# Optimization experiments

Measured on AMD Instinct MI355X. Metric: run time of the kernel, lower is better.

## Reference

```python
import jax, jax.numpy as jnp
import numpy as np

N = 50000
E = 800000
IN_DIM = 128
HID = 128


def setup_inputs() -> dict:
    key = jax.random.key(0)
    ks = jax.random.split(key, 8)
    x = jax.random.normal(ks[0], (N, IN_DIM), dtype=jnp.float32)
    edge_index = jax.random.randint(ks[1], (2, E), 0, N, dtype=jnp.int64)
    s1 = 1.0 / np.sqrt(IN_DIM)
    s2 = 1.0 / np.sqrt(HID)
    Wl1 = jax.random.uniform(ks[2], (HID, IN_DIM), jnp.float32, -s1, s1)
    bl1 = jnp.zeros((HID,), jnp.float32)
    Wr1 = jax.random.uniform(ks[3], (HID, IN_DIM), jnp.float32, -s1, s1)
    Wl2 = jax.random.uniform(ks[4], (HID, HID), jnp.float32, -s2, s2)
    bl2 = jnp.zeros((HID,), jnp.float32)
    Wr2 = jax.random.uniform(ks[5], (HID, HID), jnp.float32, -s2, s2)
    return {"x": x, "Wl1": Wl1, "bl1": bl1, "Wr1": Wr1,
            "Wl2": Wl2, "bl2": bl2, "Wr2": Wr2, "edge_index": edge_index}


def _sage_layer(h, src, dst, deg_inv, Wl, bl, Wr):
    # mean aggregation over in-edges: gather source feats, scatter-sum to targets
    msg_sum = jax.ops.segment_sum(h[src], dst, num_segments=N)  # [N, d]
    agg = msg_sum * deg_inv[:, None]
    return agg @ Wl.T + bl + h @ Wr.T


def reference(x, Wl1, bl1, Wr1, Wl2, bl2, Wr2, edge_index):
    src, dst = edge_index[0], edge_index[1]
    deg = jax.ops.segment_sum(jnp.ones((E,), x.dtype), dst, num_segments=N)
    deg_inv = 1.0 / jnp.maximum(deg, 1.0)
    h = jax.nn.relu(_sage_layer(x, src, dst, deg_inv, Wl1, bl1, Wr1))
    h = jax.nn.relu(_sage_layer(h, src, dst, deg_inv, Wl2, bl2, Wr2))
    return h  # dropout is identity in eval mode
```

## Files before the change

### kernel.cpp

```cpp
#include <hip/hip_runtime.h>

#define N_NODES 50000
#define N_ROWS_PAD 50064
#define N_EDGES 800000
#define DIM 128
#define KCAT 256
#define CAP 64

#define PACK_N (2 * DIM * KCAT)
#define CAST_N (N_NODES * 16)
#define FILL_N N_EDGES
#define PREP_TOTAL (PACK_N + CAST_N + FILL_N)

typedef unsigned int u32;
typedef unsigned short u16;
typedef __attribute__((ext_vector_type(8))) short short8;
typedef __attribute__((ext_vector_type(4))) float f32x4;

static __device__ __forceinline__ u16 f2bf(float f) {
  union { float f; u32 u; } v; v.f = f;
  u32 r = v.u + 0x7fffu + ((v.u >> 16) & 1u);
  return (u16)(r >> 16);
}
static __device__ __forceinline__ float bflo(u32 p) { return __uint_as_float(p << 16); }
static __device__ __forceinline__ float bfhi(u32 p) { return __uint_as_float(p & 0xffff0000u); }

__global__ void prep(const float* __restrict__ wl1, const float* __restrict__ wr1,
                     const float* __restrict__ wl2, const float* __restrict__ wr2,
                     const float* __restrict__ x,
                     const int* __restrict__ src, const int* __restrict__ dst,
                     int* __restrict__ cnt, u16* __restrict__ csr,
                     u16* __restrict__ wcat, u32* __restrict__ abuf) {
  int idx = blockIdx.x * blockDim.x + threadIdx.x;
  if (idx < PACK_N) {
    int layer = idx >> 15;
    int n = (idx >> 8) & 127;
    int k = idx & 255;
    const float* wl = layer ? wl2 : wl1;
    const float* wr = layer ? wr2 : wr1;
    float v = (k < DIM) ? wl[n * DIM + k] : wr[n * DIM + (k - DIM)];
    wcat[idx] = f2bf(v);
  } else if (idx < PACK_N + CAST_N) {
    int t = idx - PACK_N;
    int node = t >> 4, q = t & 15;
    float4 v0 = ((const float4*)x)[(size_t)node * 32 + q * 2];
    float4 v1 = ((const float4*)x)[(size_t)node * 32 + q * 2 + 1];
    uint4 p;
    p.x = (u32)f2bf(v0.x) | ((u32)f2bf(v0.y) << 16);
    p.y = (u32)f2bf(v0.z) | ((u32)f2bf(v0.w) << 16);
    p.z = (u32)f2bf(v1.x) | ((u32)f2bf(v1.y) << 16);
    p.w = (u32)f2bf(v1.z) | ((u32)f2bf(v1.w) << 16);
    ((uint4*)abuf)[(size_t)node * 32 + 16 + q] = p;
  } else {
    int e = idx - (PACK_N + CAST_N);
    if (e < N_EDGES) {
      int d = dst[e];
      int pos = atomicAdd(&cnt[d], 1);
      if (pos < CAP) csr[(size_t)pos * N_NODES + d] = (u16)src[e];
    }
  }
}

__global__ __launch_bounds__(256) void aggregate(
    u32* __restrict__ abuf, const u16* __restrict__ csr,
    const int* __restrict__ cnt) {
  int wid = (blockIdx.x * blockDim.x + threadIdx.x) >> 6;
  if (wid >= N_NODES) return;
  int lane = threadIdx.x & 63;
  int sub = lane >> 4, q = lane & 15;
  int craw = cnt[wid];
  int c = min(craw, CAP);
  const u16* col = csr + wid;
  const uint4* h16 = (const uint4*)abuf;
  float a0 = 0, a1 = 0, a2 = 0, a3 = 0, a4 = 0, a5 = 0, a6 = 0, a7 = 0;
#define ACC8(u) { a0 += bflo(u.x); a1 += bfhi(u.x); a2 += bflo(u.y); a3 += bfhi(u.y); \
                  a4 += bflo(u.z); a5 += bfhi(u.z); a6 += bflo(u.w); a7 += bfhi(u.w); }
  int i = sub;
  for (; i + 12 < c; i += 16) {
    u32 s0 = col[(size_t)i * N_NODES];
    u32 s1 = col[(size_t)(i + 4) * N_NODES];
    u32 s2 = col[(size_t)(i + 8) * N_NODES];
    u32 s3 = col[(size_t)(i + 12) * N_NODES];
    uint4 u0 = h16[(size_t)s0 * 32 + 16 + q];
    uint4 u1 = h16[(size_t)s1 * 32 + 16 + q];
    uint4 u2 = h16[(size_t)s2 * 32 + 16 + q];
    uint4 u3 = h16[(size_t)s3 * 32 + 16 + q];
    ACC8(u0); ACC8(u1); ACC8(u2); ACC8(u3);
  }
  for (; i < c; i += 4) {
    uint4 u0 = h16[(size_t)((u32)col[(size_t)i * N_NODES]) * 32 + 16 + q];
    ACC8(u0);
  }
#undef ACC8
  a0 += __shfl_xor(a0, 16); a1 += __shfl_xor(a1, 16);
  a2 += __shfl_xor(a2, 16); a3 += __shfl_xor(a3, 16);
  a4 += __shfl_xor(a4, 16); a5 += __shfl_xor(a5, 16);
  a6 += __shfl_xor(a6, 16); a7 += __shfl_xor(a7, 16);
  a0 += __shfl_xor(a0, 32); a1 += __shfl_xor(a1, 32);
  a2 += __shfl_xor(a2, 32); a3 += __shfl_xor(a3, 32);
  a4 += __shfl_xor(a4, 32); a5 += __shfl_xor(a5, 32);
  a6 += __shfl_xor(a6, 32); a7 += __shfl_xor(a7, 32);
  if (lane < 16) {
    float di = 1.0f / (float)max(craw, 1);
    uint4 p;
    p.x = (u32)f2bf(a0 * di) | ((u32)f2bf(a1 * di) << 16);
    p.y = (u32)f2bf(a2 * di) | ((u32)f2bf(a3 * di) << 16);
    p.z = (u32)f2bf(a4 * di) | ((u32)f2bf(a5 * di) << 16);
    p.w = (u32)f2bf(a6 * di) | ((u32)f2bf(a7 * di) << 16);
    ((uint4*)abuf)[(size_t)wid * 32 + q] = p;
  }
}

__global__ __launch_bounds__(256) void dense_mfma(
    const u16* __restrict__ abuf, const u16* __restrict__ wcat,
    const float* __restrict__ bias, float* __restrict__ fout,
    u16* __restrict__ bout) {
  const int lane = threadIdx.x & 63;
  const int wv = threadIdx.x >> 6;
  const int row0 = blockIdx.x * 64 + wv * 16;
  const int l15 = lane & 15;
  const int koff = (lane >> 4) * 8;

  const short8* ap = (const short8*)(abuf + (size_t)(row0 + l15) * KCAT + koff);
  const short8* bp = (const short8*)(wcat + (size_t)l15 * KCAT + koff);

  f32x4 acc[8];
#pragma unroll
  for (int t = 0; t < 8; ++t) acc[t] = (f32x4){0.f, 0.f, 0.f, 0.f};

#pragma unroll
  for (int ks = 0; ks < 8; ++ks) {
    short8 a = ap[ks * 4];
#pragma unroll
    for (int nt = 0; nt < 8; ++nt) {
      short8 b = bp[nt * 512 + ks * 4];
      acc[nt] = __builtin_amdgcn_mfma_f32_16x16x32_bf16(a, b, acc[nt], 0, 0, 0);
    }
  }

  const int rbase = row0 + ((lane >> 4) << 2);
#pragma unroll
  for (int nt = 0; nt < 8; ++nt) {
    int col = nt * 16 + l15;
    float bb = bias[col];
#pragma unroll
    for (int r = 0; r < 4; ++r) {
      int row = rbase + r;
      if (row < N_NODES) {
        float v = fmaxf(acc[nt][r] + bb, 0.f);
        if (fout) fout[(size_t)row * DIM + col] = v;
        if (bout) bout[(size_t)row * KCAT + DIM + col] = f2bf(v);
      }
    }
  }
}

extern "C" void kernel_launch(void* const* d_in, const int* in_sizes, int n_in,
                              void* d_out, int out_size, void* d_ws, size_t ws_size,
                              hipStream_t stream) {
  const float* x   = (const float*)d_in[0];
  const float* Wl1 = (const float*)d_in[1];
  const float* bl1 = (const float*)d_in[2];
  const float* Wr1 = (const float*)d_in[3];
  const float* Wl2 = (const float*)d_in[4];
  const float* bl2 = (const float*)d_in[5];
  const float* Wr2 = (const float*)d_in[6];
  const int* eidx  = (const int*)d_in[7];
  const int* src = eidx;
  const int* dst = eidx + N_EDGES;
  float* out = (float*)d_out;

  char* ws = (char*)d_ws;
  int* cnt  = (int*)ws;
  u16* csr  = (u16*)(ws + 256 * 1024);
  u16* wcat = (u16*)(ws + 6815744);
  u16* abuf = (u16*)(ws + 6946816);

  hipMemsetAsync(cnt, 0, N_NODES * sizeof(int), stream);

  prep<<<PREP_TOTAL / 256, 256, 0, stream>>>(Wl1, Wr1, Wl2, Wr2, x, src, dst,
                                             cnt, csr, wcat, (u32*)abuf);

  const int agg_grid = (N_NODES * 64 + 255) / 256;
  const int dense_grid = N_ROWS_PAD / 64;

  aggregate<<<agg_grid, 256, 0, stream>>>((u32*)abuf, csr, cnt);
  dense_mfma<<<dense_grid, 256, 0, stream>>>(abuf, wcat, bl1, (float*)nullptr, abuf);

  aggregate<<<agg_grid, 256, 0, stream>>>((u32*)abuf, csr, cnt);
  dense_mfma<<<dense_grid, 256, 0, stream>>>(abuf, wcat + DIM * KCAT, bl2, out,
                                             (u16*)nullptr);
}
```

Baseline: 271.0 us.

## Fuse neighbor aggregation into MFMA dense layer via shared-memory staging

Merges the aggregate and dense_mfma kernels into one fused_layer kernel. Each wavefront aggregates its 16 rows into LDS and then feeds them straight into the MFMA, so the aggregated half of the concatenated activation buffer no longer round-trips through global memory. Features are split into separate x and h buffers with a 128-wide pitch, and the CSR fill uses nontemporal stores. The cost is fewer waves in flight during the latency-bound gather: one wave now handles 16 nodes serially, where before each node had its own wave.

```diff
diff --git a/kernel.cpp b/kernel.cpp
--- a/kernel.cpp
+++ b/kernel.cpp
@@ -6,11 +6,11 @@
 #define DIM 128
 #define KCAT 256
 #define CAP 64
+#define MPITCH 264
 
 #define PACK_N (2 * DIM * KCAT)
 #define CAST_N (N_NODES * 16)
-#define FILL_N N_EDGES
-#define PREP_TOTAL (PACK_N + CAST_N + FILL_N)
+#define PREP_TOTAL (PACK_N + CAST_N + N_EDGES)
 
 typedef unsigned int u32;
 typedef unsigned short u16;
@@ -30,7 +30,7 @@
                      const float* __restrict__ x,
                      const int* __restrict__ src, const int* __restrict__ dst,
                      int* __restrict__ cnt, u16* __restrict__ csr,
-                     u16* __restrict__ wcat, u32* __restrict__ abuf) {
+                     u16* __restrict__ wcat, u32* __restrict__ bufx) {
   int idx = blockIdx.x * blockDim.x + threadIdx.x;
   if (idx < PACK_N) {
     int layer = idx >> 15;
@@ -50,106 +50,115 @@
     p.y = (u32)f2bf(v0.z) | ((u32)f2bf(v0.w) << 16);
     p.z = (u32)f2bf(v1.x) | ((u32)f2bf(v1.y) << 16);
     p.w = (u32)f2bf(v1.z) | ((u32)f2bf(v1.w) << 16);
-    ((uint4*)abuf)[(size_t)node * 32 + 16 + q] = p;
+    ((uint4*)bufx)[(size_t)node * 16 + q] = p;
   } else {
     int e = idx - (PACK_N + CAST_N);
     if (e < N_EDGES) {
       int d = dst[e];
       int pos = atomicAdd(&cnt[d], 1);
-      if (pos < CAP) csr[(size_t)pos * N_NODES + d] = (u16)src[e];
-    }
-  }
-}
-
-__global__ __launch_bounds__(256) void aggregate(
-    u32* __restrict__ abuf, const u16* __restrict__ csr,
-    const int* __restrict__ cnt) {
-  int wid = (blockIdx.x * blockDim.x + threadIdx.x) >> 6;
-  if (wid >= N_NODES) return;
-  int lane = threadIdx.x & 63;
-  int sub = lane >> 4, q = lane & 15;
-  int craw = cnt[wid];
-  int c = min(craw, CAP);
-  const u16* col = csr + wid;
-  const uint4* h16 = (const uint4*)abuf;
-  float a0 = 0, a1 = 0, a2 = 0, a3 = 0, a4 = 0, a5 = 0, a6 = 0, a7 = 0;
-#define ACC8(u) { a0 += bflo(u.x); a1 += bfhi(u.x); a2 += bflo(u.y); a3 += bfhi(u.y); \
-                  a4 += bflo(u.z); a5 += bfhi(u.z); a6 += bflo(u.w); a7 += bfhi(u.w); }
-  int i = sub;
-  for (; i + 12 < c; i += 16) {
-    u32 s0 = col[(size_t)i * N_NODES];
-    u32 s1 = col[(size_t)(i + 4) * N_NODES];
-    u32 s2 = col[(size_t)(i + 8) * N_NODES];
-    u32 s3 = col[(size_t)(i + 12) * N_NODES];
-    uint4 u0 = h16[(size_t)s0 * 32 + 16 + q];
-    uint4 u1 = h16[(size_t)s1 * 32 + 16 + q];
-    uint4 u2 = h16[(size_t)s2 * 32 + 16 + q];
-    uint4 u3 = h16[(size_t)s3 * 32 + 16 + q];
-    ACC8(u0); ACC8(u1); ACC8(u2); ACC8(u3);
-  }
-  for (; i < c; i += 4) {
-    uint4 u0 = h16[(size_t)((u32)col[(size_t)i * N_NODES]) * 32 + 16 + q];
-    ACC8(u0);
-  }
-#undef ACC8
-  a0 += __shfl_xor(a0, 16); a1 += __shfl_xor(a1, 16);
-  a2 += __shfl_xor(a2, 16); a3 += __shfl_xor(a3, 16);
-  a4 += __shfl_xor(a4, 16); a5 += __shfl_xor(a5, 16);
-  a6 += __shfl_xor(a6, 16); a7 += __shfl_xor(a7, 16);
-  a0 += __shfl_xor(a0, 32); a1 += __shfl_xor(a1, 32);
-  a2 += __shfl_xor(a2, 32); a3 += __shfl_xor(a3, 32);
-  a4 += __shfl_xor(a4, 32); a5 += __shfl_xor(a5, 32);
-  a6 += __shfl_xor(a6, 32); a7 += __shfl_xor(a7, 32);
-  if (lane < 16) {
-    float di = 1.0f / (float)max(craw, 1);
-    uint4 p;
-    p.x = (u32)f2bf(a0 * di) | ((u32)f2bf(a1 * di) << 16);
-    p.y = (u32)f2bf(a2 * di) | ((u32)f2bf(a3 * di) << 16);
-    p.z = (u32)f2bf(a4 * di) | ((u32)f2bf(a5 * di) << 16);
-    p.w = (u32)f2bf(a6 * di) | ((u32)f2bf(a7 * di) << 16);
-    ((uint4*)abuf)[(size_t)wid * 32 + q] = p;
-  }
-}
-
-__global__ __launch_bounds__(256) void dense_mfma(
-    const u16* __restrict__ abuf, const u16* __restrict__ wcat,
+      if (pos < CAP)
+        __builtin_nontemporal_store((u16)src[e], &csr[(size_t)pos * N_NODES + d]);
+    }
+  }
+}
+
+__global__ __launch_bounds__(256) void fused_layer(
+    const u16* __restrict__ hin, const u16* __restrict__ csr,
+    const int* __restrict__ cnt, const u16* __restrict__ wcat,
     const float* __restrict__ bias, float* __restrict__ fout,
     u16* __restrict__ bout) {
+  __shared__ u16 smsg[4 * 16 * MPITCH];
   const int lane = threadIdx.x & 63;
   const int wv = threadIdx.x >> 6;
   const int row0 = blockIdx.x * 64 + wv * 16;
+  const int sub = lane >> 4, q = lane & 15;
+  const uint4* h16 = (const uint4*)hin;
+  u16* msgw = smsg + wv * 16 * MPITCH;
+
+  for (int r = 0; r < 16; ++r) {
+    int node = row0 + r;
+    if (node >= N_NODES) break;
+    int craw = cnt[node];
+    int c = min(craw, CAP);
+    const u16* col = csr + node;
+    float a0 = 0, a1 = 0, a2 = 0, a3 = 0, a4 = 0, a5 = 0, a6 = 0, a7 = 0;
+#define ACC8(u) { a0 += bflo(u.x); a1 += bfhi(u.x); a2 += bflo(u.y); a3 += bfhi(u.y); \
+                  a4 += bflo(u.z); a5 += bfhi(u.z); a6 += bflo(u.w); a7 += bfhi(u.w); }
+    int i = sub;
+    for (; i + 12 < c; i += 16) {
+      u32 s0 = col[(size_t)i * N_NODES];
+      u32 s1 = col[(size_t)(i + 4) * N_NODES];
+      u32 s2 = col[(size_t)(i + 8) * N_NODES];
+      u32 s3 = col[(size_t)(i + 12) * N_NODES];
+      uint4 u0 = h16[(size_t)s0 * 16 + q];
+      uint4 u1 = h16[(size_t)s1 * 16 + q];
+      uint4 u2 = h16[(size_t)s2 * 16 + q];
+      uint4 u3 = h16[(size_t)s3 * 16 + q];
+      ACC8(u0); ACC8(u1); ACC8(u2); ACC8(u3);
+    }
+    for (; i < c; i += 4) {
+      uint4 u0 = h16[(size_t)((u32)col[(size_t)i * N_NODES]) * 16 + q];
+      ACC8(u0);
+    }
+#undef ACC8
+    a0 += __shfl_xor(a0, 16); a1 += __shfl_xor(a1, 16);
+    a2 += __shfl_xor(a2, 16); a3 += __shfl_xor(a3, 16);
+    a4 += __shfl_xor(a4, 16); a5 += __shfl_xor(a5, 16);
+    a6 += __shfl_xor(a6, 16); a7 += __shfl_xor(a7, 16);
+    a0 += __shfl_xor(a0, 32); a1 += __shfl_xor(a1, 32);
+    a2 += __shfl_xor(a2, 32); a3 += __shfl_xor(a3, 32);
+    a4 += __shfl_xor(a4, 32); a5 += __shfl_xor(a5, 32);
+    a6 += __shfl_xor(a6, 32); a7 += __shfl_xor(a7, 32);
+    if (lane < 16) {
+      float di = 1.0f / (float)max(craw, 1);
+      uint4 p;
+      p.x = (u32)f2bf(a0 * di) | ((u32)f2bf(a1 * di) << 16);
+      p.y = (u32)f2bf(a2 * di) | ((u32)f2bf(a3 * di) << 16);
+      p.z = (u32)f2bf(a4 * di) | ((u32)f2bf(a5 * di) << 16);
+      p.w = (u32)f2bf(a6 * di) | ((u32)f2bf(a7 * di) << 16);
+      *(uint4*)&msgw[r * MPITCH + q * 8] = p;
+    }
+  }
+  __syncthreads();
+
   const int l15 = lane & 15;
-  const int koff = (lane >> 4) * 8;
-
-  const short8* ap = (const short8*)(abuf + (size_t)(row0 + l15) * KCAT + koff);
-  const short8* bp = (const short8*)(wcat + (size_t)l15 * KCAT + koff);
+  const int ch = lane >> 4;
+  const short8* bp = (const short8*)(wcat + (size_t)l15 * KCAT + ch * 8);
 
   f32x4 acc[8];
 #pragma unroll
   for (int t = 0; t < 8; ++t) acc[t] = (f32x4){0.f, 0.f, 0.f, 0.f};
 
 #pragma unroll
-  for (int ks = 0; ks < 8; ++ks) {
+  for (int ks = 0; ks < 4; ++ks) {
+    short8 a = *(const short8*)&msgw[l15 * MPITCH + ch * 8 + ks * 32];
+#pragma unroll
+    for (int nt = 0; nt < 8; ++nt)
+      acc[nt] = __builtin_amdgcn_mfma_f32_16x16x32_bf16(a, bp[nt * 512 + ks * 4],
+                                                        acc[nt], 0, 0, 0);
+  }
+  const short8* ap = (const short8*)(hin + (size_t)(row0 + l15) * DIM + ch * 8);
+#pragma unroll
+  for (int ks = 0; ks < 4; ++ks) {
     short8 a = ap[ks * 4];
 #pragma unroll
-    for (int nt = 0; nt < 8; ++nt) {
-      short8 b = bp[nt * 512 + ks * 4];
-      acc[nt] = __builtin_amdgcn_mfma_f32_16x16x32_bf16(a, b, acc[nt], 0, 0, 0);
-    }
-  }
-
-  const int rbase = row0 + ((lane >> 4) << 2);
+    for (int nt = 0; nt < 8; ++nt)
+      acc[nt] = __builtin_amdgcn_mfma_f32_16x16x32_bf16(
+          a, bp[nt * 512 + (4 + ks) * 4], acc[nt], 0, 0, 0);
+  }
+
+  const int rbase = row0 + (ch << 2);
 #pragma unroll
   for (int nt = 0; nt < 8; ++nt) {
-    int col = nt * 16 + l15;
-    float bb = bias[col];
+    int colj = nt * 16 + l15;
+    float bb = bias[colj];
 #pragma unroll
     for (int r = 0; r < 4; ++r) {
       int row = rbase + r;
       if (row < N_NODES) {
         float v = fmaxf(acc[nt][r] + bb, 0.f);
-        if (fout) fout[(size_t)row * DIM + col] = v;
-        if (bout) bout[(size_t)row * KCAT + DIM + col] = f2bf(v);
+        if (fout) fout[(size_t)row * DIM + colj] = v;
+        if (bout) bout[(size_t)row * DIM + colj] = f2bf(v);
       }
     }
   }
@@ -174,20 +183,18 @@
   int* cnt  = (int*)ws;
   u16* csr  = (u16*)(ws + 256 * 1024);
   u16* wcat = (u16*)(ws + 6815744);
-  u16* abuf = (u16*)(ws + 6946816);
+  u16* bufx = (u16*)(ws + 6946816);
+  u16* bufh = (u16*)(ws + 19763200);
 
   hipMemsetAsync(cnt, 0, N_NODES * sizeof(int), stream);
 
   prep<<<PREP_TOTAL / 256, 256, 0, stream>>>(Wl1, Wr1, Wl2, Wr2, x, src, dst,
-                                             cnt, csr, wcat, (u32*)abuf);
-
-  const int agg_grid = (N_NODES * 64 + 255) / 256;
-  const int dense_grid = N_ROWS_PAD / 64;
-
-  aggregate<<<agg_grid, 256, 0, stream>>>((u32*)abuf, csr, cnt);
-  dense_mfma<<<dense_grid, 256, 0, stream>>>(abuf, wcat, bl1, (float*)nullptr, abuf);
-
-  aggregate<<<agg_grid, 256, 0, stream>>>((u32*)abuf, csr, cnt);
-  dense_mfma<<<dense_grid, 256, 0, stream>>>(abuf, wcat + DIM * KCAT, bl2, out,
-                                             (u16*)nullptr);
-}
+                                             cnt, csr, wcat, (u32*)bufx);
+
+  const int grid = N_ROWS_PAD / 64;
+
+  fused_layer<<<grid, 256, 0, stream>>>(bufx, csr, cnt, wcat, bl1,
+                                        (float*)nullptr, bufh);
+  fused_layer<<<grid, 256, 0, stream>>>(bufh, csr, cnt, wcat + DIM * KCAT, bl2,
+                                        out, (u16*)nullptr);
+}
```

Measured after the change: 320.3 us. +18.2%, slower.
